# Kernel tuning notes

Hardware: AMD Instinct MI355X
Metric: run time of the kernel (lower is better)

The kernel has to match this reference:

```python
import jax, jax.numpy as jnp
import numpy as np

PI = 3.14159265358979323846
MARGIN = 6.0
DIM = 256
ENT_TOT = 43234
REL_RANGE = (6.0 + 2.0) / DIM  # (margin + epsilon) / dim = 0.03125


def setup_inputs() -> dict:
    key = jax.random.key(0)
    k1, k2, k3 = jax.random.split(key, 3)
    head = jax.random.normal(k1, (32, 2 * DIM), dtype=jnp.float32)
    relation = jax.random.normal(k2, (32, DIM), dtype=jnp.float32)
    ent_emb = jax.random.normal(k3, (ENT_TOT, 2 * DIM), dtype=jnp.float32)
    return {"head": head, "relation": relation, "ent_emb": ent_emb}


def reference(head, relation, ent_emb):
    # head: (B, 2D) -> re/im halves (B, D)
    re_h, im_h = jnp.split(head, 2, axis=-1)
    # entity table: (E, 2D) -> (E, D) each
    re_t, im_t = jnp.split(ent_emb, 2, axis=-1)
    # phase rotation from relation embedding
    phase = relation / (REL_RANGE / PI)          # (B, D)
    re_r = jnp.cos(phase)
    im_r = jnp.sin(phase)
    # complex rotation of head by relation: (B, D)
    re_rot = re_h * re_r - im_h * im_r
    im_rot = re_h * im_r + im_h * re_r
    # difference against every entity, broadcast to (B, E, D)
    re_s = re_rot[:, None, :] - re_t[None, :, :]
    im_s = im_rot[:, None, :] - im_t[None, :, :]
    # L2 norm over the complex pair, summed over D -> (B, E)
    dist = jnp.sqrt(re_s * re_s + im_s * im_s).sum(axis=-1)
    return MARGIN - dist
```

## Files before the change

kernel.cpp:

```cpp
#include <hip/hip_runtime.h>
#include <math.h>

#define DIMH 256
#define NB   32
#define E_TOT 43234
#define TE   32
#define DK   32
#define NC   (DIMH / DK)

typedef float v2f __attribute__((ext_vector_type(2)));
typedef float v4f __attribute__((ext_vector_type(4)));

__global__ __launch_bounds__(64) void rot_kernel(const float* __restrict__ head,
                                                 const float* __restrict__ rel,
                                                 float4* __restrict__ rot_v4) {
    int i  = blockIdx.x * 64 + threadIdx.x;
    int b  = i >> 7;
    int dp = i & 127;
    int d0 = dp * 2;
    float4 w;
    {
        float re_h = head[b * 2 * DIMH + d0];
        float im_h = head[b * 2 * DIMH + DIMH + d0];
        float x = rel[b * DIMH + d0] * 16.0f;
        float f = x - floorf(x);
        float s = __builtin_amdgcn_sinf(f);
        float c = __builtin_amdgcn_cosf(f);
        w.x = re_h * c - im_h * s;
        w.z = re_h * s + im_h * c;
    }
    {
        float re_h = head[b * 2 * DIMH + d0 + 1];
        float im_h = head[b * 2 * DIMH + DIMH + d0 + 1];
        float x = rel[b * DIMH + d0 + 1] * 16.0f;
        float f = x - floorf(x);
        float s = __builtin_amdgcn_sinf(f);
        float c = __builtin_amdgcn_cosf(f);
        w.y = re_h * c - im_h * s;
        w.w = re_h * s + im_h * c;
    }
    rot_v4[b * (DIMH / 2) + dp] = w;
}

__device__ __forceinline__ v2f sqrt2(v2f s) {
    v2f r;
    r.x = __builtin_amdgcn_sqrtf(s.x);
    r.y = __builtin_amdgcn_sqrtf(s.y);
    return r;
}

__global__ __launch_bounds__(64, 2) void dist_kernel(const float* __restrict__ ent,
                                                     const float4* __restrict__ rot_v4,
                                                     float* __restrict__ out) {
    __shared__ v4f s_e[TE][16];
    __shared__ v4f s_r[NB][16];

    const int tid = threadIdx.x;
    const int eb  = blockIdx.x * TE;
    const int eg  = tid & 7;
    const int bg  = tid >> 3;

    const int erow = tid >> 3;
    const int eq   = tid & 7;
    const int rrow = tid >> 4;
    const int rcol = tid & 15;

    float4 pe_re[4], pe_im[4], pr[8];

    auto load_chunk = [&](int c) {
        const int dk = c * DK;
        #pragma unroll
        for (int k = 0; k < 4; ++k) {
            int er = min(eb + 8 * k + erow, E_TOT - 1);
            const float* b0 = ent + (size_t)er * (2 * DIMH);
            pe_re[k] = *reinterpret_cast<const float4*>(b0 + dk + 4 * eq);
            pe_im[k] = *reinterpret_cast<const float4*>(b0 + DIMH + dk + 4 * eq);
        }
        #pragma unroll
        for (int k = 0; k < 8; ++k)
            pr[k] = rot_v4[(4 * k + rrow) * (DIMH / 2) + c * (DK / 2) + rcol];
    };

    auto store_chunk = [&]() {
        #pragma unroll
        for (int k = 0; k < 4; ++k) {
            int row = 8 * k + erow;
            int s = (row >> 2) & 7;
            v4f lo, hi;
            lo.x = pe_re[k].x; lo.y = pe_re[k].y; lo.z = pe_im[k].x; lo.w = pe_im[k].y;
            hi.x = pe_re[k].z; hi.y = pe_re[k].w; hi.z = pe_im[k].z; hi.w = pe_im[k].w;
            s_e[row][(2 * eq)     ^ s] = lo;
            s_e[row][(2 * eq + 1) ^ s] = hi;
        }
        #pragma unroll
        for (int k = 0; k < 8; ++k) {
            int row = 4 * k + rrow;
            int s = (row >> 2) & 7;
            v4f r; r.x = pr[k].x; r.y = pr[k].y; r.z = pr[k].z; r.w = pr[k].w;
            s_r[row][rcol ^ s] = r;
        }
    };

    v2f acc[4][4];
    #pragma unroll
    for (int j = 0; j < 4; ++j)
        #pragma unroll
        for (int k = 0; k < 4; ++k) { acc[j][k].x = 0.f; acc[j][k].y = 0.f; }

    load_chunk(0);

    #pragma unroll 1
    for (int c = 0; c < NC; ++c) {
        store_chunk();
        if (c + 1 < NC) load_chunk(c + 1);

        #pragma unroll 4
        for (int p = 0; p < DK / 2; ++p) {
            v4f r0 = s_r[4 * bg + 0][p ^ bg];
            v4f r1 = s_r[4 * bg + 1][p ^ bg];
            v4f r2 = s_r[4 * bg + 2][p ^ bg];
            v4f r3 = s_r[4 * bg + 3][p ^ bg];
            v4f e0 = s_e[4 * eg + 0][p ^ eg];
            v4f e1 = s_e[4 * eg + 1][p ^ eg];
            v4f e2 = s_e[4 * eg + 2][p ^ eg];
            v4f e3 = s_e[4 * eg + 3][p ^ eg];
            #define CONTRIB(J, K, R, E)                         \
                { v2f a = R.xy - E.xy; v2f b = R.zw - E.zw;     \
                  acc[J][K] += sqrt2(a * a + b * b); }
            CONTRIB(0,0,r0,e0) CONTRIB(0,1,r0,e1) CONTRIB(0,2,r0,e2) CONTRIB(0,3,r0,e3)
            CONTRIB(1,0,r1,e0) CONTRIB(1,1,r1,e1) CONTRIB(1,2,r1,e2) CONTRIB(1,3,r1,e3)
            CONTRIB(2,0,r2,e0) CONTRIB(2,1,r2,e1) CONTRIB(2,2,r2,e2) CONTRIB(2,3,r2,e3)
            CONTRIB(3,0,r3,e0) CONTRIB(3,1,r3,e1) CONTRIB(3,2,r3,e2) CONTRIB(3,3,r3,e3)
            #undef CONTRIB
        }
    }

    #pragma unroll
    for (int j = 0; j < 4; ++j) {
        int b = 4 * bg + j;
        float v0 = 6.0f - (acc[j][0].x + acc[j][0].y);
        float v1 = 6.0f - (acc[j][1].x + acc[j][1].y);
        float v2 = 6.0f - (acc[j][2].x + acc[j][2].y);
        float v3 = 6.0f - (acc[j][3].x + acc[j][3].y);
        int e4 = eb + 4 * eg;
        float* op = out + (size_t)b * E_TOT + e4;
        if (e4 + 3 < E_TOT) {
            float2 w0; w0.x = v0; w0.y = v1;
            float2 w1; w1.x = v2; w1.y = v3;
            *reinterpret_cast<float2*>(op)     = w0;
            *reinterpret_cast<float2*>(op + 2) = w1;
        } else {
            if (e4     < E_TOT) op[0] = v0;
            if (e4 + 1 < E_TOT) op[1] = v1;
            if (e4 + 2 < E_TOT) op[2] = v2;
            if (e4 + 3 < E_TOT) op[3] = v3;
        }
    }
}

extern "C" void kernel_launch(void* const* d_in, const int* in_sizes, int n_in,
                              void* d_out, int out_size, void* d_ws, size_t ws_size,
                              hipStream_t stream) {
    const float* head = (const float*)d_in[0];
    const float* rel  = (const float*)d_in[1];
    const float* ent  = (const float*)d_in[2];
    float4* rot_v4 = (float4*)d_ws;

    rot_kernel<<<(NB * DIMH / 2) / 64, 64, 0, stream>>>(head, rel, rot_v4);

    int etiles = (E_TOT + TE - 1) / TE;
    dist_kernel<<<etiles, 64, 0, stream>>>(ent, rot_v4, (float*)d_out);
}
```

Baseline: 195.7 us.

## Split reduction dimension across four wavefronts per block with LDS reduction

Each block now runs four wavefronts, each covering a quarter of the 256-wide embedding dimension in 16-wide chunks, and their partial sums are combined through shared memory before output. The goal is more wavefronts per entity tile, giving better latency hiding and occupancy without changing the tile shape. The cost is a shared-memory reduction with two barriers, scalar instead of vectorized output stores, and shorter per-wave pipelines.

```diff
diff --git a/kernel.cpp b/kernel.cpp
--- a/kernel.cpp
+++ b/kernel.cpp
@@ -5,8 +5,8 @@
 #define NB   32
 #define E_TOT 43234
 #define TE   32
-#define DK   32
-#define NC   (DIMH / DK)
+#define DK   16
+#define NCW  4
 
 typedef float v2f __attribute__((ext_vector_type(2)));
 typedef float v4f __attribute__((ext_vector_type(4)));
@@ -49,55 +49,61 @@
     return r;
 }
 
-__global__ __launch_bounds__(64, 2) void dist_kernel(const float* __restrict__ ent,
-                                                     const float4* __restrict__ rot_v4,
-                                                     float* __restrict__ out) {
-    __shared__ v4f s_e[TE][16];
-    __shared__ v4f s_r[NB][16];
+__global__ __launch_bounds__(256, 5) void dist_kernel(const float* __restrict__ ent,
+                                                      const float4* __restrict__ rot_v4,
+                                                      float* __restrict__ out) {
+    __shared__ v4f smem[2048];
 
-    const int tid = threadIdx.x;
-    const int eb  = blockIdx.x * TE;
-    const int eg  = tid & 7;
-    const int bg  = tid >> 3;
+    const int tid  = threadIdx.x;
+    const int lane = tid & 63;
+    const int w    = tid >> 6;
+    const int eb   = blockIdx.x * TE;
+    const int eg   = lane & 7;
+    const int bg   = lane >> 3;
 
-    const int erow = tid >> 3;
-    const int eq   = tid & 7;
-    const int rrow = tid >> 4;
-    const int rcol = tid & 15;
+    v4f* se = smem + w * 512;
+    v4f* sr = se + 256;
 
-    float4 pe_re[4], pe_im[4], pr[8];
+    const int erow = lane >> 2;
+    const int eq   = lane & 3;
+    const int rb   = lane >> 3;
+    const int rdpi = lane & 7;
+
+    const int c0 = w * NCW;
+
+    float4 pe_re[2], pe_im[2], pr[4];
 
     auto load_chunk = [&](int c) {
         const int dk = c * DK;
         #pragma unroll
-        for (int k = 0; k < 4; ++k) {
-            int er = min(eb + 8 * k + erow, E_TOT - 1);
+        for (int s = 0; s < 2; ++s) {
+            int er = min(eb + erow + 16 * s, E_TOT - 1);
             const float* b0 = ent + (size_t)er * (2 * DIMH);
-            pe_re[k] = *reinterpret_cast<const float4*>(b0 + dk + 4 * eq);
-            pe_im[k] = *reinterpret_cast<const float4*>(b0 + DIMH + dk + 4 * eq);
+            pe_re[s] = *reinterpret_cast<const float4*>(b0 + dk + 4 * eq);
+            pe_im[s] = *reinterpret_cast<const float4*>(b0 + DIMH + dk + 4 * eq);
         }
         #pragma unroll
-        for (int k = 0; k < 8; ++k)
-            pr[k] = rot_v4[(4 * k + rrow) * (DIMH / 2) + c * (DK / 2) + rcol];
+        for (int s = 0; s < 4; ++s)
+            pr[s] = rot_v4[(rb + 8 * s) * (DIMH / 2) + c * (DK / 2) + rdpi];
     };
 
     auto store_chunk = [&]() {
         #pragma unroll
-        for (int k = 0; k < 4; ++k) {
-            int row = 8 * k + erow;
-            int s = (row >> 2) & 7;
+        for (int s = 0; s < 2; ++s) {
+            int row = erow + 16 * s;
+            int sw  = row >> 2;
             v4f lo, hi;
-            lo.x = pe_re[k].x; lo.y = pe_re[k].y; lo.z = pe_im[k].x; lo.w = pe_im[k].y;
-            hi.x = pe_re[k].z; hi.y = pe_re[k].w; hi.z = pe_im[k].z; hi.w = pe_im[k].w;
-            s_e[row][(2 * eq)     ^ s] = lo;
-            s_e[row][(2 * eq + 1) ^ s] = hi;
+            lo.x = pe_re[s].x; lo.y = pe_re[s].y; lo.z = pe_im[s].x; lo.w = pe_im[s].y;
+            hi.x = pe_re[s].z; hi.y = pe_re[s].w; hi.z = pe_im[s].z; hi.w = pe_im[s].w;
+            se[row * 8 + ((2 * eq)     ^ sw)] = lo;
+            se[row * 8 + ((2 * eq + 1) ^ sw)] = hi;
         }
         #pragma unroll
-        for (int k = 0; k < 8; ++k) {
-            int row = 4 * k + rrow;
-            int s = (row >> 2) & 7;
-            v4f r; r.x = pr[k].x; r.y = pr[k].y; r.z = pr[k].z; r.w = pr[k].w;
-            s_r[row][rcol ^ s] = r;
+        for (int s = 0; s < 4; ++s) {
+            int b  = rb + 8 * s;
+            int sw = b >> 2;
+            v4f r; r.x = pr[s].x; r.y = pr[s].y; r.z = pr[s].z; r.w = pr[s].w;
+            sr[b * 8 + (rdpi ^ sw)] = r;
         }
     };
 
@@ -107,23 +113,24 @@
         #pragma unroll
         for (int k = 0; k < 4; ++k) { acc[j][k].x = 0.f; acc[j][k].y = 0.f; }
 
-    load_chunk(0);
+    load_chunk(c0);
 
     #pragma unroll 1
-    for (int c = 0; c < NC; ++c) {
+    for (int cc = 0; cc < NCW; ++cc) {
         store_chunk();
-        if (c + 1 < NC) load_chunk(c + 1);
+        if (cc + 1 < NCW) load_chunk(c0 + cc + 1);
 
         #pragma unroll 4
         for (int p = 0; p < DK / 2; ++p) {
-            v4f r0 = s_r[4 * bg + 0][p ^ bg];
-            v4f r1 = s_r[4 * bg + 1][p ^ bg];
-            v4f r2 = s_r[4 * bg + 2][p ^ bg];
-            v4f r3 = s_r[4 * bg + 3][p ^ bg];
-            v4f e0 = s_e[4 * eg + 0][p ^ eg];
-            v4f e1 = s_e[4 * eg + 1][p ^ eg];
-            v4f e2 = s_e[4 * eg + 2][p ^ eg];
-            v4f e3 = s_e[4 * eg + 3][p ^ eg];
+            int pe = p ^ eg, pb = p ^ bg;
+            v4f r0 = sr[(4 * bg + 0) * 8 + pb];
+            v4f r1 = sr[(4 * bg + 1) * 8 + pb];
+            v4f r2 = sr[(4 * bg + 2) * 8 + pb];
+            v4f r3 = sr[(4 * bg + 3) * 8 + pb];
+            v4f e0 = se[(4 * eg + 0) * 8 + pe];
+            v4f e1 = se[(4 * eg + 1) * 8 + pe];
+            v4f e2 = se[(4 * eg + 2) * 8 + pe];
+            v4f e3 = se[(4 * eg + 3) * 8 + pe];
             #define CONTRIB(J, K, R, E)                         \
                 { v2f a = R.xy - E.xy; v2f b = R.zw - E.zw;     \
                   acc[J][K] += sqrt2(a * a + b * b); }
@@ -135,25 +142,34 @@
         }
     }
 
+    float part[16];
     #pragma unroll
-    for (int j = 0; j < 4; ++j) {
-        int b = 4 * bg + j;
-        float v0 = 6.0f - (acc[j][0].x + acc[j][0].y);
-        float v1 = 6.0f - (acc[j][1].x + acc[j][1].y);
-        float v2 = 6.0f - (acc[j][2].x + acc[j][2].y);
-        float v3 = 6.0f - (acc[j][3].x + acc[j][3].y);
-        int e4 = eb + 4 * eg;
-        float* op = out + (size_t)b * E_TOT + e4;
-        if (e4 + 3 < E_TOT) {
-            float2 w0; w0.x = v0; w0.y = v1;
-            float2 w1; w1.x = v2; w1.y = v3;
-            *reinterpret_cast<float2*>(op)     = w0;
-            *reinterpret_cast<float2*>(op + 2) = w1;
-        } else {
-            if (e4     < E_TOT) op[0] = v0;
-            if (e4 + 1 < E_TOT) op[1] = v1;
-            if (e4 + 2 < E_TOT) op[2] = v2;
-            if (e4 + 3 < E_TOT) op[3] = v3;
+    for (int j = 0; j < 4; ++j)
+        #pragma unroll
+        for (int k = 0; k < 4; ++k)
+            part[j * 4 + k] = acc[j][k].x + acc[j][k].y;
+
+    __syncthreads();
+    float* red = (float*)smem;
+    #pragma unroll
+    for (int i = 0; i < 16; ++i)
+        red[tid * 17 + i] = part[i];
+    __syncthreads();
+
+    #pragma unroll
+    for (int t = 0; t < 4; ++t) {
+        int O  = tid + 256 * t;
+        int b  = O >> 5;
+        int ei = O & 31;
+        int e  = eb + ei;
+        if (e < E_TOT) {
+            int lane_src = ((b >> 2) << 3) + (ei >> 2);
+            int idx      = ((b & 3) << 2) + (ei & 3);
+            float sum = red[(0 * 64 + lane_src) * 17 + idx]
+                      + red[(1 * 64 + lane_src) * 17 + idx]
+                      + red[(2 * 64 + lane_src) * 17 + idx]
+                      + red[(3 * 64 + lane_src) * 17 + idx];
+            out[(size_t)b * E_TOT + e] = 6.0f - sum;
         }
     }
 }
@@ -169,5 +185,5 @@
     rot_kernel<<<(NB * DIMH / 2) / 64, 64, 0, stream>>>(head, rel, rot_v4);
 
     int etiles = (E_TOT + TE - 1) / TE;
-    dist_kernel<<<etiles, 64, 0, stream>>>(ent, rot_v4, (float*)d_out);
+    dist_kernel<<<etiles, 256, 0, stream>>>(ent, rot_v4, (float*)d_out);
 }
```

After: 212.6 us. 8.6% more time.
